# Kernel tuning notes

Hardware: AMD Instinct MI355X
Metric: run time of the kernel (lower is better)

## Reference

```python
import jax, jax.numpy as jnp
import numpy as np
import math

B, L, D, H = 4, 1024, 1024, 16
HD = D // H  # head dim = 64


def setup_inputs() -> dict:
    key = jax.random.key(0)
    ks = jax.random.split(key, 8)
    s = 1.0 / math.sqrt(D)
    return {
        "Q": jax.random.normal(ks[0], (B, L, D), jnp.float32),
        "K": jax.random.normal(ks[1], (B, L, D), jnp.float32),
        "V": jax.random.normal(ks[2], (B, L, D), jnp.float32),
        "valid_lens": jax.random.randint(ks[3], (B * H * L,), 0, L, jnp.int32),
        "Wq": jax.random.normal(ks[4], (D, D), jnp.float32) * s,
        "Wk": jax.random.normal(ks[5], (D, D), jnp.float32) * s,
        "Wv": jax.random.normal(ks[6], (D, D), jnp.float32) * s,
        "Wo": jax.random.normal(ks[7], (D, D), jnp.float32) * s,
    }


def _split_heads(X):
    # [B, L, D] -> [B*H, L, HD]
    return X.reshape(B, L, H, HD).transpose(0, 2, 1, 3).reshape(B * H, L, HD)


def reference(Q, K, V, valid_lens, Wq, Wk, Wv, Wo):
    q = _split_heads(Q @ Wq.T)
    k = _split_heads(K @ Wk.T)
    v = _split_heads(V @ Wv.T)
    # scaled dot-product scores: [B*H, Lq, Lk]
    scores = jnp.einsum("bqd,bkd->bqk", q, k) / math.sqrt(HD)
    # original flattens scores to [B*H*Lq, Lk] and masks with a
    # [len(valid_lens), Lq] mask (Lq == Lk here) of -1e6, then softmax
    mask = jnp.arange(L)[None, :] < valid_lens[:, None]  # [B*H*L, L]
    flat = jnp.where(mask, scores.reshape(-1, L), jnp.float32(-1e6))
    attn = jax.nn.softmax(flat, axis=-1).reshape(B * H, L, L)
    out = jnp.einsum("bqk,bkd->bqd", attn, v)  # dropout p=0 is identity
    # merge heads: [B*H, L, HD] -> [B, L, D]
    out = out.reshape(B, H, L, HD).transpose(0, 2, 1, 3).reshape(B, L, D)
    return out @ Wo.T
```

## Files before the change

kernel.cpp:

```cpp
#include <hip/hip_runtime.h>
#include <hip/hip_bf16.h>

typedef short v8s __attribute__((ext_vector_type(8)));
typedef unsigned short v8u __attribute__((ext_vector_type(8)));
typedef float v4f __attribute__((ext_vector_type(4)));
typedef unsigned short u16;

#define LL 1024
#define DD 1024

static __device__ __forceinline__ u16 f2b(float x) {
  __hip_bfloat16 h = __float2bfloat16(x);
  return __builtin_bit_cast(u16, h);
}

static __device__ __forceinline__ void gload_lds16(const u16* g, u16* l) {
  __builtin_amdgcn_global_load_lds((const __attribute__((address_space(1))) void*)g,
                                   (__attribute__((address_space(3))) void*)l, 16, 0, 0);
}

__global__ __launch_bounds__(256) void cvt3(const float* __restrict__ p0,
                                            const float* __restrict__ p1,
                                            const float* __restrict__ p2,
                                            u16* __restrict__ out, int n8, long ostride) {
  const float* src = blockIdx.y == 0 ? p0 : (blockIdx.y == 1 ? p1 : p2);
  u16* dst = out + (long)blockIdx.y * ostride;
  int i = blockIdx.x * 256 + threadIdx.x;
  if (i >= n8) return;
  const float4* p = (const float4*)src + (long)i * 2;
  float4 a = p[0], b = p[1];
  v8u r;
  r[0] = f2b(a.x); r[1] = f2b(a.y); r[2] = f2b(a.z); r[3] = f2b(a.w);
  r[4] = f2b(b.x); r[5] = f2b(b.y); r[6] = f2b(b.z); r[7] = f2b(b.w);
  *((v8u*)dst + i) = r;
}

template <typename OUTT>
__global__ __launch_bounds__(256) void gemm_bt(const u16* __restrict__ A,
                                               const u16* __restrict__ Bw,
                                               OUTT* __restrict__ C,
                                               long za, long zb, long zc) {
  __shared__ u16 As[128 * 64];
  __shared__ u16 Bs[128 * 64];
  A += (long)blockIdx.z * za;
  Bw += (long)blockIdx.z * zb;
  C += (long)blockIdx.z * zc;
  const int tid = threadIdx.x;
  const int lane = tid & 63;
  const int l15 = lane & 15, lg = lane >> 4;
  const int wid = tid >> 6;
  const int wm = wid >> 1, wn = wid & 1;
  const long mbase = (long)blockIdx.y * 128;
  const long nbase = (long)blockIdx.x * 128;

  const u16* ap = A + (mbase + (tid >> 3)) * 1024 + (tid & 7) * 8;
  const u16* bp = Bw + (nbase + (tid >> 3)) * 1024 + (tid & 7) * 8;

  v4f acc[4][4] = {};

  for (int kt = 0; kt < 16; ++kt) {
    __syncthreads();
#pragma unroll
    for (int j = 0; j < 4; ++j) {
      gload_lds16(ap + kt * 64 + j * 32 * 1024, &As[(tid + 256 * j) * 8]);
      gload_lds16(bp + kt * 64 + j * 32 * 1024, &Bs[(tid + 256 * j) * 8]);
    }
    __syncthreads();
#pragma unroll
    for (int kk = 0; kk < 2; ++kk) {
      v8s a[4], b[4];
#pragma unroll
      for (int i = 0; i < 4; ++i)
        a[i] = *(const v8s*)&As[(wm * 64 + i * 16 + l15) * 64 + kk * 32 + lg * 8];
#pragma unroll
      for (int i = 0; i < 4; ++i)
        b[i] = *(const v8s*)&Bs[(wn * 64 + i * 16 + l15) * 64 + kk * 32 + lg * 8];
#pragma unroll
      for (int mi = 0; mi < 4; ++mi)
#pragma unroll
        for (int nj = 0; nj < 4; ++nj)
          acc[mi][nj] = __builtin_amdgcn_mfma_f32_16x16x32_bf16(a[mi], b[nj], acc[mi][nj], 0, 0, 0);
    }
  }
#pragma unroll
  for (int mi = 0; mi < 4; ++mi) {
#pragma unroll
    for (int r = 0; r < 4; ++r) {
      long row = mbase + wm * 64 + mi * 16 + lg * 4 + r;
#pragma unroll
      for (int nj = 0; nj < 4; ++nj) {
        long col = nbase + wn * 64 + nj * 16 + l15;
        if constexpr (__is_same(OUTT, float))
          C[row * 1024 + col] = acc[mi][nj][r];
        else
          C[row * 1024 + col] = f2b(acc[mi][nj][r]);
      }
    }
  }
}

__global__ __launch_bounds__(256) void attn_kern(const u16* __restrict__ qb,
                                                 const u16* __restrict__ kb,
                                                 const u16* __restrict__ vb,
                                                 const int* __restrict__ valid,
                                                 u16* __restrict__ ob) {
  __shared__ u16 Ks[64 * 72];
  __shared__ u16 Vt[64 * 72];
  __shared__ u16 Ps[4][16 * 72];
  __shared__ int s_mv;

  const int tid = threadIdx.x;
  const int lane = tid & 63;
  const int wid = tid >> 6;
  const int l15 = lane & 15, lg = lane >> 4;
  const int bh = blockIdx.y;
  const int b = bh >> 4, h = bh & 15;
  const int qrow0 = blockIdx.x * 64 + wid * 16;
  const long headoff = ((long)b * LL) * DD + h * 64;

  v8s qf[2];
#pragma unroll
  for (int ks = 0; ks < 2; ++ks)
    qf[ks] = *(const v8s*)(qb + headoff + (long)(qrow0 + l15) * DD + ks * 32 + lg * 8);

  int vraw[4];
  int mymax = 1;
#pragma unroll
  for (int r = 0; r < 4; ++r) {
    int v = valid[bh * LL + qrow0 + lg * 4 + r];
    vraw[r] = v;
    mymax = max(mymax, v == 0 ? LL : v);
  }
  if (tid == 0) s_mv = 1;
  int wmax = mymax;
#pragma unroll
  for (int d = 1; d < 64; d <<= 1) wmax = max(wmax, __shfl_xor(wmax, d));
  __syncthreads();
  if (lane == 0) atomicMax(&s_mv, wmax);
  __syncthreads();
  const int ntiles = (s_mv + 63) >> 6;

  float mrow[4], lrow[4];
  v4f oacc[4] = {};
#pragma unroll
  for (int r = 0; r < 4; ++r) { mrow[r] = -1e30f; lrow[r] = 0.0f; }

  const int kk = tid & 63;
  const int qtr = tid >> 6;

  for (int kt = 0; kt < ntiles; ++kt) {
    __syncthreads();
    {
      const long rowoff = headoff + (long)(kt * 64 + kk) * DD + qtr * 16;
      v8s k0 = *(const v8s*)(kb + rowoff);
      v8s k1 = *(const v8s*)(kb + rowoff + 8);
      v8s v0 = *(const v8s*)(vb + rowoff);
      v8s v1 = *(const v8s*)(vb + rowoff + 8);
      *(v8s*)&Ks[kk * 72 + qtr * 16] = k0;
      *(v8s*)&Ks[kk * 72 + qtr * 16 + 8] = k1;
      v8u u0 = __builtin_bit_cast(v8u, v0);
      v8u u1 = __builtin_bit_cast(v8u, v1);
#pragma unroll
      for (int j = 0; j < 8; ++j) Vt[(qtr * 16 + j) * 72 + kk] = u0[j];
#pragma unroll
      for (int j = 0; j < 8; ++j) Vt[(qtr * 16 + 8 + j) * 72 + kk] = u1[j];
    }
    __syncthreads();

    v4f s[4];
#pragma unroll
    for (int t = 0; t < 4; ++t) {
      v4f z = {};
#pragma unroll
      for (int ks = 0; ks < 2; ++ks) {
        v8s kf = *(const v8s*)&Ks[(t * 16 + l15) * 72 + ks * 32 + lg * 8];
        z = __builtin_amdgcn_mfma_f32_16x16x32_bf16(qf[ks], kf, z, 0, 0, 0);
      }
      s[t] = z;
    }

    const int colbase = kt * 64 + l15;
#pragma unroll
    for (int t = 0; t < 4; ++t)
#pragma unroll
      for (int r = 0; r < 4; ++r) {
        float val = s[t][r] * 0.125f;
        s[t][r] = (colbase + t * 16 < vraw[r]) ? val : -1e6f;
      }

    float pm[4];
#pragma unroll
    for (int r = 0; r < 4; ++r)
      pm[r] = fmaxf(fmaxf(s[0][r], s[1][r]), fmaxf(s[2][r], s[3][r]));
#pragma unroll
    for (int d = 1; d < 16; d <<= 1)
#pragma unroll
      for (int r = 0; r < 4; ++r) pm[r] = fmaxf(pm[r], __shfl_xor(pm[r], d));

    float sc[4];
#pragma unroll
    for (int r = 0; r < 4; ++r) {
      float mn = fmaxf(mrow[r], pm[r]);
      sc[r] = __expf(mrow[r] - mn);
      mrow[r] = mn;
    }
    float rs[4] = {0.f, 0.f, 0.f, 0.f};
#pragma unroll
    for (int t = 0; t < 4; ++t)
#pragma unroll
      for (int r = 0; r < 4; ++r) {
        float p = __expf(s[t][r] - mrow[r]);
        s[t][r] = p;
        rs[r] += p;
      }
#pragma unroll
    for (int d = 1; d < 16; d <<= 1)
#pragma unroll
      for (int r = 0; r < 4; ++r) rs[r] += __shfl_xor(rs[r], d);
#pragma unroll
    for (int r = 0; r < 4; ++r) lrow[r] = lrow[r] * sc[r] + rs[r];
#pragma unroll
    for (int t = 0; t < 4; ++t)
#pragma unroll
      for (int r = 0; r < 4; ++r) oacc[t][r] *= sc[r];

#pragma unroll
    for (int t = 0; t < 4; ++t)
#pragma unroll
      for (int r = 0; r < 4; ++r)
        Ps[wid][(lg * 4 + r) * 72 + t * 16 + l15] = f2b(s[t][r]);

    asm volatile("s_waitcnt lgkmcnt(0)" ::: "memory");
    __builtin_amdgcn_sched_barrier(0);

#pragma unroll
    for (int ks = 0; ks < 2; ++ks) {
      v8s pa = *(const v8s*)&Ps[wid][l15 * 72 + ks * 32 + lg * 8];
#pragma unroll
      for (int t = 0; t < 4; ++t) {
        v8s vf = *(const v8s*)&Vt[(t * 16 + l15) * 72 + ks * 32 + lg * 8];
        oacc[t] = __builtin_amdgcn_mfma_f32_16x16x32_bf16(pa, vf, oacc[t], 0, 0, 0);
      }
    }
  }

#pragma unroll
  for (int r = 0; r < 4; ++r) {
    float inv = 1.0f / lrow[r];
    long rp = headoff + (long)(qrow0 + lg * 4 + r) * DD;
#pragma unroll
    for (int t = 0; t < 4; ++t)
      ob[rp + t * 16 + l15] = f2b(oacc[t][r] * inv);
  }
}

extern "C" void kernel_launch(void* const* d_in, const int* in_sizes, int n_in,
                              void* d_out, int out_size, void* d_ws, size_t ws_size,
                              hipStream_t stream) {
  const float* Q = (const float*)d_in[0];
  const float* K = (const float*)d_in[1];
  const float* V = (const float*)d_in[2];
  const int* valid = (const int*)d_in[3];
  const float* Wq = (const float*)d_in[4];
  const float* Wk = (const float*)d_in[5];
  const float* Wv = (const float*)d_in[6];
  const float* Wo = (const float*)d_in[7];
  float* out = (float*)d_out;

  u16* ws = (u16*)d_ws;
  const long MK = 4096L * 1024;
  const long NK = 1024L * 1024;
  u16* qkvb = ws;
  u16* wqkv = qkvb + 3 * MK;
  u16* wo = wqkv + 3 * NK;
  u16* proj = wo + NK;
  u16* ob = proj + 3 * MK;

  cvt3<<<dim3(2048, 3), 256, 0, stream>>>(Q, K, V, qkvb, (int)(MK / 8), MK);
  cvt3<<<dim3(512, 3), 256, 0, stream>>>(Wq, Wk, Wv, wqkv, (int)(NK / 8), NK);
  cvt3<<<dim3(512, 1), 256, 0, stream>>>(Wo, Wo, Wo, wo, (int)(NK / 8), 0);

  gemm_bt<u16><<<dim3(8, 32, 3), 256, 0, stream>>>(qkvb, wqkv, proj, MK, NK, MK);
  attn_kern<<<dim3(16, 64), 256, 0, stream>>>(proj, proj + MK, proj + 2 * MK, valid, ob);
  gemm_bt<float><<<dim3(8, 32, 1), 256, 0, stream>>>(ob, wo, out, 0, 0, 0);
}
```

Before: 154.1 us.

## Sort query rows by valid length per head to cut masked key tiles

Adds a per-head counting-sort kernel that orders query rows by valid length and writes a permutation into the spent input workspace. Each attention block then handles 64 rows with similar lengths, so the number of key tiles it visits is set by its own group maximum rather than by a mixed group. The change also skips the online-softmax rescale when the running max grows by at most 8, and raises wave priority around the MFMA sections. In exchange there is one extra small kernel launch, gathered Q loads and output stores, and load imbalance across blocks.

```diff
diff --git a/kernel.cpp b/kernel.cpp
--- a/kernel.cpp
+++ b/kernel.cpp
@@ -33,6 +33,49 @@
   r[0] = f2b(a.x); r[1] = f2b(a.y); r[2] = f2b(a.z); r[3] = f2b(a.w);
   r[4] = f2b(b.x); r[5] = f2b(b.y); r[6] = f2b(b.z); r[7] = f2b(b.w);
   *((v8u*)dst + i) = r;
+}
+
+__global__ __launch_bounds__(256) void sortperm(const int* __restrict__ valid,
+                                                u16* __restrict__ perm) {
+  __shared__ int hist[1024];
+  __shared__ int wsum[4];
+  const int bh = blockIdx.x;
+  const int tid = threadIdx.x;
+  const int* v = valid + bh * 1024;
+  for (int i = tid; i < 1024; i += 256) hist[i] = 0;
+  __syncthreads();
+  for (int i = tid; i < 1024; i += 256) {
+    int k = v[i];
+    k = (k == 0) ? 1023 : (k - 1);
+    atomicAdd(&hist[k], 1);
+  }
+  __syncthreads();
+  const int base = tid * 4;
+  int h0 = hist[base], h1 = hist[base + 1], h2 = hist[base + 2], h3 = hist[base + 3];
+  int local = h0 + h1 + h2 + h3;
+  const int lane = tid & 63, w = tid >> 6;
+  int scan = local;
+#pragma unroll
+  for (int d = 1; d < 64; d <<= 1) {
+    int t = __shfl_up(scan, d);
+    if (lane >= d) scan += t;
+  }
+  if (lane == 63) wsum[w] = scan;
+  __syncthreads();
+  int woff = 0;
+  for (int i = 0; i < w; ++i) woff += wsum[i];
+  int excl = woff + scan - local;
+  hist[base] = excl;
+  hist[base + 1] = excl + h0;
+  hist[base + 2] = excl + h0 + h1;
+  hist[base + 3] = excl + h0 + h1 + h2;
+  __syncthreads();
+  for (int i = tid; i < 1024; i += 256) {
+    int k = v[i];
+    k = (k == 0) ? 1023 : (k - 1);
+    int pos = atomicAdd(&hist[k], 1);
+    perm[bh * 1024 + pos] = (u16)i;
+  }
 }
 
 template <typename OUTT>
@@ -103,11 +146,11 @@
                                                  const u16* __restrict__ kb,
                                                  const u16* __restrict__ vb,
                                                  const int* __restrict__ valid,
+                                                 const u16* __restrict__ perm,
                                                  u16* __restrict__ ob) {
   __shared__ u16 Ks[64 * 72];
   __shared__ u16 Vt[64 * 72];
   __shared__ u16 Ps[4][16 * 72];
-  __shared__ int s_mv;
 
   const int tid = threadIdx.x;
   const int lane = tid & 63;
@@ -115,30 +158,25 @@
   const int l15 = lane & 15, lg = lane >> 4;
   const int bh = blockIdx.y;
   const int b = bh >> 4, h = bh & 15;
-  const int qrow0 = blockIdx.x * 64 + wid * 16;
   const long headoff = ((long)b * LL) * DD + h * 64;
-
+  const u16* pblk = perm + bh * 1024 + blockIdx.x * 64;
+  const u16* pp = pblk + wid * 16;
+
+  const int qrowA = pp[l15];
   v8s qf[2];
 #pragma unroll
   for (int ks = 0; ks < 2; ++ks)
-    qf[ks] = *(const v8s*)(qb + headoff + (long)(qrow0 + l15) * DD + ks * 32 + lg * 8);
-
-  int vraw[4];
-  int mymax = 1;
+    qf[ks] = *(const v8s*)(qb + headoff + (long)qrowA * DD + ks * 32 + lg * 8);
+
+  int orow[4], vraw[4];
 #pragma unroll
   for (int r = 0; r < 4; ++r) {
-    int v = valid[bh * LL + qrow0 + lg * 4 + r];
-    vraw[r] = v;
-    mymax = max(mymax, v == 0 ? LL : v);
-  }
-  if (tid == 0) s_mv = 1;
-  int wmax = mymax;
-#pragma unroll
-  for (int d = 1; d < 64; d <<= 1) wmax = max(wmax, __shfl_xor(wmax, d));
-  __syncthreads();
-  if (lane == 0) atomicMax(&s_mv, wmax);
-  __syncthreads();
-  const int ntiles = (s_mv + 63) >> 6;
+    int rr = pp[lg * 4 + r];
+    orow[r] = rr;
+    vraw[r] = valid[bh * LL + rr];
+  }
+  const int lastv = valid[bh * LL + pblk[63]];
+  const int ntiles = ((lastv == 0 ? LL : lastv) + 63) >> 6;
 
   float mrow[4], lrow[4];
   v4f oacc[4] = {};
@@ -168,6 +206,7 @@
     __syncthreads();
 
     v4f s[4];
+    __builtin_amdgcn_s_setprio(1);
 #pragma unroll
     for (int t = 0; t < 4; ++t) {
       v4f z = {};
@@ -178,6 +217,7 @@
       }
       s[t] = z;
     }
+    __builtin_amdgcn_s_setprio(0);
 
     const int colbase = kt * 64 + l15;
 #pragma unroll
@@ -197,12 +237,19 @@
 #pragma unroll
       for (int r = 0; r < 4; ++r) pm[r] = fmaxf(pm[r], __shfl_xor(pm[r], d));
 
-    float sc[4];
-#pragma unroll
-    for (int r = 0; r < 4; ++r) {
-      float mn = fmaxf(mrow[r], pm[r]);
-      sc[r] = __expf(mrow[r] - mn);
-      mrow[r] = mn;
+    bool sk = true;
+#pragma unroll
+    for (int r = 0; r < 4; ++r) sk = sk && (pm[r] <= mrow[r] + 8.0f);
+    if (!__all(sk)) {
+#pragma unroll
+      for (int r = 0; r < 4; ++r) {
+        float mn = fmaxf(mrow[r], pm[r]);
+        float sc = __expf(mrow[r] - mn);
+        mrow[r] = mn;
+        lrow[r] *= sc;
+#pragma unroll
+        for (int t = 0; t < 4; ++t) oacc[t][r] *= sc;
+      }
     }
     float rs[4] = {0.f, 0.f, 0.f, 0.f};
 #pragma unroll
@@ -218,11 +265,7 @@
 #pragma unroll
       for (int r = 0; r < 4; ++r) rs[r] += __shfl_xor(rs[r], d);
 #pragma unroll
-    for (int r = 0; r < 4; ++r) lrow[r] = lrow[r] * sc[r] + rs[r];
-#pragma unroll
-    for (int t = 0; t < 4; ++t)
-#pragma unroll
-      for (int r = 0; r < 4; ++r) oacc[t][r] *= sc[r];
+    for (int r = 0; r < 4; ++r) lrow[r] += rs[r];
 
 #pragma unroll
     for (int t = 0; t < 4; ++t)
@@ -233,6 +276,7 @@
     asm volatile("s_waitcnt lgkmcnt(0)" ::: "memory");
     __builtin_amdgcn_sched_barrier(0);
 
+    __builtin_amdgcn_s_setprio(1);
 #pragma unroll
     for (int ks = 0; ks < 2; ++ks) {
       v8s pa = *(const v8s*)&Ps[wid][l15 * 72 + ks * 32 + lg * 8];
@@ -242,12 +286,13 @@
         oacc[t] = __builtin_amdgcn_mfma_f32_16x16x32_bf16(pa, vf, oacc[t], 0, 0, 0);
       }
     }
+    __builtin_amdgcn_s_setprio(0);
   }
 
 #pragma unroll
   for (int r = 0; r < 4; ++r) {
     float inv = 1.0f / lrow[r];
-    long rp = headoff + (long)(qrow0 + lg * 4 + r) * DD;
+    long rp = headoff + (long)orow[r] * DD;
 #pragma unroll
     for (int t = 0; t < 4; ++t)
       ob[rp + t * 16 + l15] = f2b(oacc[t][r] * inv);
@@ -275,12 +320,14 @@
   u16* wo = wqkv + 3 * NK;
   u16* proj = wo + NK;
   u16* ob = proj + 3 * MK;
+  u16* perm = qkvb;
 
   cvt3<<<dim3(2048, 3), 256, 0, stream>>>(Q, K, V, qkvb, (int)(MK / 8), MK);
   cvt3<<<dim3(512, 3), 256, 0, stream>>>(Wq, Wk, Wv, wqkv, (int)(NK / 8), NK);
   cvt3<<<dim3(512, 1), 256, 0, stream>>>(Wo, Wo, Wo, wo, (int)(NK / 8), 0);
 
   gemm_bt<u16><<<dim3(8, 32, 3), 256, 0, stream>>>(qkvb, wqkv, proj, MK, NK, MK);
-  attn_kern<<<dim3(16, 64), 256, 0, stream>>>(proj, proj + MK, proj + 2 * MK, valid, ob);
+  sortperm<<<64, 256, 0, stream>>>(valid, perm);
+  attn_kern<<<dim3(16, 64), 256, 0, stream>>>(proj, proj + MK, proj + 2 * MK, valid, perm, ob);
   gemm_bt<float><<<dim3(8, 32, 1), 256, 0, stream>>>(ob, wo, out, 0, 0, 0);
 }
```

After: 156.2 us. Within noise of the previous version (+1.4%).
